# Optimization experiments

Hardware: AMD Instinct MI355X
Metric: run time of the kernel (lower is better)

The kernel has to match this reference:

```python
import jax, jax.numpy as jnp
import numpy as np

MAX_DISP = 48


def setup_inputs() -> dict:
    key = jax.random.key(0)
    k1, k2 = jax.random.split(key)
    left = jax.random.normal(k1, (2, 64, 256, 32), dtype=jnp.float32)
    right = jax.random.normal(k2, (2, 64, 256, 32), dtype=jnp.float32)
    return {"left": left, "right": right}


def reference(left, right):
    # left, right: [B, H, W, C] NHWC feature maps.
    # For each disparity d in [-D, D): out[b, d+D, h, w] = concat(left[b,h,w], right[b,h,w-d])
    # where positions with (w - d) out of [0, W) are zeroed (matches TF concat+pad semantics:
    # the pad zeroes BOTH the left and right channel halves in the invalid region).
    B, H, W, C = left.shape
    disps = jnp.arange(-MAX_DISP, MAX_DISP)          # [2D]
    w_idx = jnp.arange(W)                            # [W]

    def level(d):
        idx = w_idx - d                              # right-image column for each output column
        valid = (idx >= 0) & (idx < W)               # [W]
        r = jnp.take(right, jnp.clip(idx, 0, W - 1), axis=2)   # [B,H,W,C]
        lvl = jnp.concatenate([left, r], axis=-1)               # [B,H,W,2C]
        return jnp.where(valid[None, None, :, None], lvl, jnp.zeros((), lvl.dtype))

    cv = jax.vmap(level)(disps)                      # [2D, B, H, W, 2C]
    return jnp.transpose(cv, (1, 0, 2, 3, 4))        # [B, 2D, H, W, 2C]
```

## Files before the change

kernel.cpp:

```cpp
#include <hip/hip_runtime.h>


typedef float f4 __attribute__((ext_vector_type(4)));

#define DD_STRIDE 262144

__global__ __launch_bounds__(256) void cost_concat_kernel(
    const f4* __restrict__ left4,
    const f4* __restrict__ right4,
    f4* __restrict__ out4)
{
    __shared__ f4 lds[2824];

    const int t   = threadIdx.x;
    const int bid = blockIdx.x;
    const int g   = bid & 1;
    const int wh  = (bid >> 1) & 1;
    const int hb  = bid >> 2;
    const int w0  = wh << 7;
    const int dd0 = g * 48;
    const int rowBase = hb * 2048;

    #pragma unroll
    for (int k = 0; k < 4; ++k)
        lds[k * 256 + t] = left4[rowBase + w0 * 8 + k * 256 + t];

    #pragma unroll
    for (int k = 0; k < 7; ++k) {
        const int q = k * 256 + t;
        const int idxPix = (w0 - 48) + (q >> 3);
        f4 v = (f4){0.f, 0.f, 0.f, 0.f};
        if ((unsigned)idxPix < 256u)
            v = right4[rowBase + idxPix * 8 + (q & 7)];
        lds[1024 + q] = v;
    }
    if (t < 8) lds[2816 + t] = (f4){0.f, 0.f, 0.f, 0.f};
    __syncthreads();

    const int c4 = t & 15;
    const int wb = t >> 4;
    const int cc = c4 & 7;
    const bool isLeft = c4 < 8;

    const int Z = 2816 * 16;
    int addrB = isLeft ? (wb * 128 + cc * 16)
                       : (16384 + (wb - dd0 + 96) * 128 + cc * 16);
    const int dec = isLeft ? 0 : 128;
    int ib = w0 + wb + 48 - dd0;

    const int b = hb >> 6, h = hb & 63;
    f4* op = out4 + (size_t)b * 25165824 + (size_t)dd0 * DD_STRIDE
                  + (size_t)h * 4096 + (size_t)(w0 * 16) + t;

    const char* ldsb = (const char*)lds;

    for (int k = 0; k < 48; ++k) {
        #pragma unroll
        for (int j = 0; j < 8; ++j) {
            const int idxj = ib + j * 16;
            const int aj   = addrB + j * 2048;
            const int sel  = ((unsigned)idxj < 256u) ? aj : Z;
            f4 v = *(const f4*)(ldsb + sel);
            __builtin_nontemporal_store(v, op + j * 256);
        }
        ib -= 1; addrB -= dec; op += DD_STRIDE;
    }
}

extern "C" void kernel_launch(void* const* d_in, const int* in_sizes, int n_in,
                              void* d_out, int out_size, void* d_ws, size_t ws_size,
                              hipStream_t stream) {
    const f4* left4  = (const f4*)d_in[0];
    const f4* right4 = (const f4*)d_in[1];
    f4* out4 = (f4*)d_out;

    cost_concat_kernel<<<512, 256, 0, stream>>>(left4, right4, out4);
}
```

Before: 155.0 us.

## Split disparity range into four blocks with 512 threads and plain stores

Each block now covers 24 disparities instead of 48, and blocks grow to 512 threads, so the grid doubles to 1024 blocks. The staged right-image window in shared memory shrinks to match, with the LDS indexing rebuilt around per-j address arrays. The nontemporal store builtin is replaced by ordinary stores. The aim is more parallelism and a smaller LDS footprint for this write-bound kernel, at the cost of reloading the left and right rows in more blocks and giving up the streaming-store hint.

```diff
diff --git a/kernel.cpp b/kernel.cpp
--- a/kernel.cpp
+++ b/kernel.cpp
@@ -5,36 +5,39 @@
 
 #define DD_STRIDE 262144
 
-__global__ __launch_bounds__(256) void cost_concat_kernel(
+__global__ __launch_bounds__(512) void cost_concat_kernel(
     const f4* __restrict__ left4,
     const f4* __restrict__ right4,
     f4* __restrict__ out4)
 {
-    __shared__ f4 lds[2824];
+    __shared__ f4 lds[2248];
 
     const int t   = threadIdx.x;
     const int bid = blockIdx.x;
-    const int g   = bid & 1;
-    const int wh  = (bid >> 1) & 1;
-    const int hb  = bid >> 2;
+    const int wh  = bid & 1;
+    const int g   = (bid >> 1) & 3;
+    const int hb  = bid >> 3;
     const int w0  = wh << 7;
-    const int dd0 = g * 48;
+    const int dd0 = g * 24;
     const int rowBase = hb * 2048;
 
     #pragma unroll
-    for (int k = 0; k < 4; ++k)
-        lds[k * 256 + t] = left4[rowBase + w0 * 8 + k * 256 + t];
+    for (int i = 0; i < 2; ++i)
+        lds[i * 512 + t] = left4[rowBase + w0 * 8 + i * 512 + t];
 
+    const int c_lo = w0 - dd0 + 25;
     #pragma unroll
-    for (int k = 0; k < 7; ++k) {
-        const int q = k * 256 + t;
-        const int idxPix = (w0 - 48) + (q >> 3);
-        f4 v = (f4){0.f, 0.f, 0.f, 0.f};
-        if ((unsigned)idxPix < 256u)
-            v = right4[rowBase + idxPix * 8 + (q & 7)];
-        lds[1024 + q] = v;
+    for (int i = 0; i < 3; ++i) {
+        const int q = i * 512 + t;
+        if (q < 1216) {
+            const int col = c_lo + (q >> 3);
+            f4 v = (f4){0.f, 0.f, 0.f, 0.f};
+            if ((unsigned)col < 256u)
+                v = right4[rowBase + col * 8 + (q & 7)];
+            lds[1024 + q] = v;
+        }
     }
-    if (t < 8) lds[2816 + t] = (f4){0.f, 0.f, 0.f, 0.f};
+    if (t < 8) lds[2240 + t] = (f4){0.f, 0.f, 0.f, 0.f};
     __syncthreads();
 
     const int c4 = t & 15;
@@ -42,28 +45,32 @@
     const int cc = c4 & 7;
     const bool isLeft = c4 < 8;
 
-    const int Z = 2816 * 16;
-    int addrB = isLeft ? (wb * 128 + cc * 16)
-                       : (16384 + (wb - dd0 + 96) * 128 + cc * 16);
+    const int Z = 2240 * 16;
+    int addr[4], idx0[4];
+    #pragma unroll
+    for (int j = 0; j < 4; ++j) {
+        addr[j] = isLeft ? ((j * 32 + wb) * 128 + cc * 16)
+                         : (16384 + (j * 32 + wb + 23) * 128 + cc * 16);
+        idx0[j] = j * 32 + wb + w0 - dd0 + 48;
+    }
     const int dec = isLeft ? 0 : 128;
-    int ib = w0 + wb + 48 - dd0;
 
     const int b = hb >> 6, h = hb & 63;
-    f4* op = out4 + (size_t)b * 25165824 + (size_t)dd0 * DD_STRIDE
-                  + (size_t)h * 4096 + (size_t)(w0 * 16) + t;
+    f4* orow = out4 + (size_t)b * 25165824 + (size_t)dd0 * DD_STRIDE
+                    + (size_t)h * 4096 + (size_t)(w0 * 16);
+    const char* lb = (const char*)lds;
 
-    const char* ldsb = (const char*)lds;
-
-    for (int k = 0; k < 48; ++k) {
+    for (int k = 0; k < 24; ++k) {
+        f4* op = orow + (size_t)k * DD_STRIDE;
         #pragma unroll
-        for (int j = 0; j < 8; ++j) {
-            const int idxj = ib + j * 16;
-            const int aj   = addrB + j * 2048;
-            const int sel  = ((unsigned)idxj < 256u) ? aj : Z;
-            f4 v = *(const f4*)(ldsb + sel);
-            __builtin_nontemporal_store(v, op + j * 256);
+        for (int j = 0; j < 4; ++j) {
+            const int idx = idx0[j] - k;
+            const int sel = ((unsigned)idx < 256u) ? addr[j] : Z;
+            f4 v = *(const f4*)(lb + sel);
+            op[j * 512 + t] = v;
         }
-        ib -= 1; addrB -= dec; op += DD_STRIDE;
+        #pragma unroll
+        for (int j = 0; j < 4; ++j) addr[j] -= dec;
     }
 }
 
@@ -74,5 +81,5 @@
     const f4* right4 = (const f4*)d_in[1];
     f4* out4 = (f4*)d_out;
 
-    cost_concat_kernel<<<512, 256, 0, stream>>>(left4, right4, out4);
+    cost_concat_kernel<<<1024, 512, 0, stream>>>(left4, right4, out4);
 }
```

Measured after the change: 150.6 us. 2.8% less time.
